# Kernel tuning notes

Measured on AMD Instinct MI355X. Metric: run time of the kernel, lower is better.

Reference implementation:

```python
import jax, jax.numpy as jnp
import numpy as np

S = 8192  # query length
T = 8192  # key/value length
D = 256   # head dim


def setup_inputs() -> dict:
    key = jax.random.key(0)
    kq, kk, kv = jax.random.split(key, 3)
    return {
        "query": jax.random.normal(kq, (S, D), dtype=jnp.float32),
        "key": jax.random.normal(kk, (T, D), dtype=jnp.float32),
        "value": jax.random.normal(kv, (T, D), dtype=jnp.float32),
    }


def reference(query, key, value):
    # attn_weights = Q @ K^T  (contract last dims, no batch dims)  -> [S, T]
    attn_weights = jnp.einsum("sd,td->st", query, key)
    # SoftmaxAttn: softmax over axes [ndim//2, ndim) == last axis for 2D
    attn_weights = jax.nn.softmax(attn_weights, axis=-1).astype(jnp.float32)
    # y = A @ V  -> [S, D]
    y = jnp.einsum("st,td->sd", attn_weights, value)
    return y
```

## Files before the change

kernel.cpp:

```cpp
#include <hip/hip_runtime.h>
#include <hip/hip_fp16.h>

#define S_LEN 8192
#define T_LEN 8192
#define D_DIM 256
#define QBLK 64
#define KVBLK 32
#define TSPLIT 8
#define NKV ((T_LEN / TSPLIT) / KVBLK)
#define NQT (S_LEN / QBLK)
#define KTILE_BYTES 16384
#define VTILE_BYTES 16384
#define RESCALE_THR 6.0f
#define LOG2E 1.44269504f

typedef _Float16 f16x8 __attribute__((ext_vector_type(8)));
typedef float f32x4 __attribute__((ext_vector_type(4)));

struct h4 { _Float16 h[4]; };

#define GLOAD_LDS16(g, l)                                              \
    __builtin_amdgcn_global_load_lds(                                  \
        (const __attribute__((address_space(1))) void*)(g),            \
        (__attribute__((address_space(3))) void*)(l), 16, 0, 0)

#define MFMA16(a, b, c) __builtin_amdgcn_mfma_f32_16x16x32_f16(a, b, c, 0, 0, 0)

#if __has_builtin(__builtin_amdgcn_exp2f)
#define EXP2(x) __builtin_amdgcn_exp2f(x)
#else
static __device__ __forceinline__ float EXP2(float x) {
    float y;
    asm("v_exp_f32 %0, %1" : "=v"(y) : "v"(x));
    return y;
}
#endif

__global__ __launch_bounds__(256) void cvt_kernel(const float* __restrict__ in,
                                                  _Float16* __restrict__ out, int n4) {
    int i = blockIdx.x * 256 + threadIdx.x;
    if (i < n4) {
        float4 v = ((const float4*)in)[i];
        h4 o;
        o.h[0] = (_Float16)(v.x * LOG2E); o.h[1] = (_Float16)(v.y * LOG2E);
        o.h[2] = (_Float16)(v.z * LOG2E); o.h[3] = (_Float16)(v.w * LOG2E);
        ((h4*)out)[i] = o;
    }
}

__global__ __launch_bounds__(256) void cvt_swz_kernel(const float* __restrict__ in,
                                                      _Float16* __restrict__ img,
                                                      int nchunks) {
    int id = blockIdx.x * 256 + threadIdx.x;
    if (id >= nchunks) return;
    int row = id >> 5, gr = id & 31;
    int t = row >> 5, r = row & 31;
    float4 a = *(const float4*)(in + (size_t)row * D_DIM + gr * 8);
    float4 b = *(const float4*)(in + (size_t)row * D_DIM + gr * 8 + 4);
    f16x8 o;
    o[0] = (_Float16)a.x; o[1] = (_Float16)a.y; o[2] = (_Float16)a.z; o[3] = (_Float16)a.w;
    o[4] = (_Float16)b.x; o[5] = (_Float16)b.y; o[6] = (_Float16)b.z; o[7] = (_Float16)b.w;
    *(f16x8*)((char*)img + (size_t)t * KTILE_BYTES + (gr >> 2) * 2048 +
              ((r >> 4) << 10) + ((r & 15) << 6) + ((gr & 3) << 4)) = o;
}

__global__ __launch_bounds__(256) void vt_swz_kernel(const float* __restrict__ V,
                                                     _Float16* __restrict__ Vimg) {
    __shared__ float tile[32][260];
    const int t = blockIdx.x;
#pragma unroll
    for (int i = 0; i < 8; ++i) {
        int idx = i * 256 + threadIdx.x;
        int kr = idx >> 6, c4 = idx & 63;
        float4 v = *(const float4*)(V + ((size_t)t * 32 + kr) * D_DIM + c4 * 4);
        tile[kr][c4 * 4 + 0] = v.x;
        tile[kr][c4 * 4 + 1] = v.y;
        tile[kr][c4 * 4 + 2] = v.z;
        tile[kr][c4 * 4 + 3] = v.w;
    }
    __syncthreads();
#pragma unroll
    for (int i = 0; i < 4; ++i) {
        int gid = i * 256 + threadIdx.x;
        int d = gid >> 2, gk = gid & 3;
        f16x8 o;
#pragma unroll
        for (int j = 0; j < 8; ++j)
            o[j] = (_Float16)tile[(j >> 2) * 16 + gk * 4 + (j & 3)][d];
        *(f16x8*)((char*)Vimg + (size_t)t * VTILE_BYTES + ((d >> 4) << 10) +
                  (gk << 8) + ((d & 15) << 4)) = o;
    }
}

__global__ __launch_bounds__(128, 2) void attn_kernel(
    const _Float16* __restrict__ Qh, const _Float16* __restrict__ Kimg,
    const _Float16* __restrict__ Vimg, _Float16* __restrict__ Opart,
    float* __restrict__ ml) {
    __shared__ __align__(16) char smem[32768];
    char* sK = smem;
    char* sV = smem + 16384;
    const int tid = threadIdx.x;
    const int wave = tid >> 6, lane = tid & 63;
    const int g = lane >> 4, c = lane & 15;
    const int qtile = blockIdx.x, split = blockIdx.y;
    const int tile0 = split * NKV;
    const int othr = tid * 16;
    const int kbase = ((lane & 15) << 6) | ((lane >> 4) << 4);
    const int vbase = lane << 4;

    f16x8 qf[2][8];
    {
        const size_t qrow0 = (size_t)qtile * QBLK + wave * 32 + c;
#pragma unroll
        for (int mi = 0; mi < 2; ++mi)
#pragma unroll
            for (int ks = 0; ks < 8; ++ks)
                qf[mi][ks] =
                    *(const f16x8*)(Qh + (qrow0 + mi * 16) * D_DIM + (ks * 4 + g) * 8);
    }

    {
        const char* Kt = (const char*)Kimg + (size_t)tile0 * KTILE_BYTES;
#pragma unroll
        for (int i = 0; i < 8; ++i) GLOAD_LDS16(Kt + i * 2048 + othr, sK + i * 2048 + othr);
    }

    f32x4 acc[2][16];
#pragma unroll
    for (int mi = 0; mi < 2; ++mi)
#pragma unroll
        for (int dt = 0; dt < 16; ++dt) acc[mi][dt] = (f32x4){0.f, 0.f, 0.f, 0.f};
    float m[2] = {-1e30f, -1e30f};
    float l[2] = {0.f, 0.f};

    for (int kt = 0; kt < NKV; ++kt) {
        asm volatile("s_waitcnt vmcnt(0)" ::: "memory");
        __builtin_amdgcn_s_barrier();

        {
            const char* Vt = (const char*)Vimg + (size_t)(tile0 + kt) * VTILE_BYTES;
#pragma unroll
            for (int i = 0; i < 8; ++i)
                GLOAD_LDS16(Vt + i * 2048 + othr, sV + i * 2048 + othr);
        }

        f32x4 st[2][2];
#pragma unroll
        for (int mi = 0; mi < 2; ++mi)
#pragma unroll
            for (int ct = 0; ct < 2; ++ct) st[mi][ct] = (f32x4){0.f, 0.f, 0.f, 0.f};
        __builtin_amdgcn_s_setprio(1);
#pragma unroll
        for (int ks = 0; ks < 8; ++ks) {
            f16x8 kf0 = *(const f16x8*)(sK + ks * 2048 + kbase);
            f16x8 kf1 = *(const f16x8*)(sK + ks * 2048 + 1024 + kbase);
            st[0][0] = MFMA16(kf0, qf[0][ks], st[0][0]);
            st[0][1] = MFMA16(kf1, qf[0][ks], st[0][1]);
            st[1][0] = MFMA16(kf0, qf[1][ks], st[1][0]);
            st[1][1] = MFMA16(kf1, qf[1][ks], st[1][1]);
        }
        __builtin_amdgcn_s_setprio(0);

        union PU { unsigned int u[4]; f16x8 v; };
        PU pu[2];
#pragma unroll
        for (int mi = 0; mi < 2; ++mi) {
            float pm = fmaxf(fmaxf(fmaxf(st[mi][0][0], st[mi][0][1]),
                                   fmaxf(st[mi][0][2], st[mi][0][3])),
                             fmaxf(fmaxf(st[mi][1][0], st[mi][1][1]),
                                   fmaxf(st[mi][1][2], st[mi][1][3])));
            if (__any(pm > m[mi] + RESCALE_THR)) {
                pm = fmaxf(pm, __shfl_xor(pm, 16));
                pm = fmaxf(pm, __shfl_xor(pm, 32));
                float mn = fmaxf(m[mi], pm);
                float sc = EXP2(m[mi] - mn);
                m[mi] = mn;
                l[mi] *= sc;
                float fr[4];
#pragma unroll
                for (int r = 0; r < 4; ++r) fr[r] = __shfl(sc, (g << 4) | (g * 4 + r));
#pragma unroll
                for (int dt = 0; dt < 16; ++dt)
#pragma unroll
                    for (int r = 0; r < 4; ++r) acc[mi][dt][r] *= fr[r];
            }
            float rs = 0.f;
#pragma unroll
            for (int ct = 0; ct < 2; ++ct)
#pragma unroll
                for (int r = 0; r < 4; ++r) {
                    float p = EXP2(st[mi][ct][r] - m[mi]);
                    st[mi][ct][r] = p;
                    rs += p;
                }
            l[mi] += rs;
            pu[mi].u[0] = __builtin_bit_cast(
                unsigned int, __builtin_amdgcn_cvt_pkrtz(st[mi][0][0], st[mi][0][1]));
            pu[mi].u[1] = __builtin_bit_cast(
                unsigned int, __builtin_amdgcn_cvt_pkrtz(st[mi][0][2], st[mi][0][3]));
            pu[mi].u[2] = __builtin_bit_cast(
                unsigned int, __builtin_amdgcn_cvt_pkrtz(st[mi][1][0], st[mi][1][1]));
            pu[mi].u[3] = __builtin_bit_cast(
                unsigned int, __builtin_amdgcn_cvt_pkrtz(st[mi][1][2], st[mi][1][3]));
        }

        asm volatile("s_waitcnt vmcnt(0)" ::: "memory");
        __builtin_amdgcn_s_barrier();

        if (kt + 1 < NKV) {
            const char* Kt = (const char*)Kimg + (size_t)(tile0 + kt + 1) * KTILE_BYTES;
#pragma unroll
            for (int i = 0; i < 8; ++i)
                GLOAD_LDS16(Kt + i * 2048 + othr, sK + i * 2048 + othr);
        }

        __builtin_amdgcn_s_setprio(1);
#pragma unroll
        for (int dt = 0; dt < 16; ++dt) {
            f16x8 vf = *(const f16x8*)(sV + dt * 1024 + vbase);
            acc[0][dt] = MFMA16(pu[0].v, vf, acc[0][dt]);
            acc[1][dt] = MFMA16(pu[1].v, vf, acc[1][dt]);
        }
        __builtin_amdgcn_s_setprio(0);
    }

    _Float16* Ob = Opart + (size_t)(qtile * TSPLIT + split) * QBLK * D_DIM;
#pragma unroll
    for (int mi = 0; mi < 2; ++mi)
#pragma unroll
        for (int dt = 0; dt < 16; ++dt)
#pragma unroll
            for (int r = 0; r < 4; ++r) {
                int row = wave * 32 + mi * 16 + g * 4 + r;
                int col = dt * 16 + c;
                Ob[(size_t)row * D_DIM + col] = (_Float16)acc[mi][dt][r];
            }
#pragma unroll
    for (int mi = 0; mi < 2; ++mi) {
        l[mi] += __shfl_xor(l[mi], 16);
        l[mi] += __shfl_xor(l[mi], 32);
    }
    if (g == 0) {
        float* mlb = ml + (size_t)((qtile * TSPLIT + split) * QBLK) * 2;
#pragma unroll
        for (int mi = 0; mi < 2; ++mi) {
            int row = wave * 32 + mi * 16 + c;
            mlb[row * 2 + 0] = m[mi];
            mlb[row * 2 + 1] = l[mi];
        }
    }
}

__global__ __launch_bounds__(256) void combine_kernel(const _Float16* __restrict__ Opart,
                                                      const float* __restrict__ ml,
                                                      float* __restrict__ out) {
    int r = blockIdx.x;
    int qtile = r >> 6, rl = r & 63;
    int d = threadIdx.x;
    float mv[TSPLIT], lv[TSPLIT];
    float M = -1e30f;
#pragma unroll
    for (int s = 0; s < TSPLIT; ++s) {
        const float* mlb = ml + (size_t)((qtile * TSPLIT + s) * QBLK + rl) * 2;
        mv[s] = mlb[0];
        lv[s] = mlb[1];
        M = fmaxf(M, mv[s]);
    }
    float num = 0.f, den = 0.f;
#pragma unroll
    for (int s = 0; s < TSPLIT; ++s) {
        float w = EXP2(mv[s] - M);
        num += w * (float)Opart[((size_t)(qtile * TSPLIT + s) * QBLK + rl) * D_DIM + d];
        den += w * lv[s];
    }
    out[(size_t)r * D_DIM + d] = num / den;
}

extern "C" void kernel_launch(void* const* d_in, const int* in_sizes, int n_in,
                              void* d_out, int out_size, void* d_ws, size_t ws_size,
                              hipStream_t stream) {
    const float* Q = (const float*)d_in[0];
    const float* K = (const float*)d_in[1];
    const float* V = (const float*)d_in[2];
    float* out = (float*)d_out;
    char* ws = (char*)d_ws;

    _Float16* Qh = (_Float16*)ws;
    _Float16* Kimg = (_Float16*)(ws + (4 << 20));
    _Float16* Vimg = (_Float16*)(ws + (8 << 20));
    _Float16* Opart = (_Float16*)(ws + (12 << 20));
    float* ml = (float*)(ws + ((size_t)44 << 20));

    const int n4 = S_LEN * D_DIM / 4;
    const int nchunks = S_LEN * D_DIM / 8;
    cvt_kernel<<<n4 / 256, 256, 0, stream>>>(Q, Qh, n4);
    cvt_swz_kernel<<<nchunks / 256, 256, 0, stream>>>(K, Kimg, nchunks);
    vt_swz_kernel<<<T_LEN / 32, 256, 0, stream>>>(V, Vimg);

    dim3 ag(NQT, TSPLIT);
    attn_kernel<<<ag, 128, 0, stream>>>(Qh, Kimg, Vimg, Opart, ml);
    combine_kernel<<<S_LEN, 256, 0, stream>>>(Opart, ml, out);
}
```

Before: 108.6 us.

## Double-buffer K/V tiles, widen Q block to 128 with rotated tile order

Raises the query block to 128 rows with 4 waves per block, so each K/V tile loaded to LDS serves twice as many queries. Replaces the serialized K-then-V load scheme with a double-buffered pipeline that prefetches the next K and V tiles together while computing the current one. Adds a per-qtile rotation of the KV tile start order and a 1D grid mapping, meant to spread concurrent block accesses across memory. LDS grows to 64KB per block, which may limit occupancy.

```diff
diff --git a/kernel.cpp b/kernel.cpp
--- a/kernel.cpp
+++ b/kernel.cpp
@@ -4,7 +4,7 @@
 #define S_LEN 8192
 #define T_LEN 8192
 #define D_DIM 256
-#define QBLK 64
+#define QBLK 128
 #define KVBLK 32
 #define TSPLIT 8
 #define NKV ((T_LEN / TSPLIT) / KVBLK)
@@ -92,18 +92,18 @@
     }
 }
 
-__global__ __launch_bounds__(128, 2) void attn_kernel(
+__global__ __launch_bounds__(256, 2) void attn_kernel(
     const _Float16* __restrict__ Qh, const _Float16* __restrict__ Kimg,
     const _Float16* __restrict__ Vimg, _Float16* __restrict__ Opart,
     float* __restrict__ ml) {
-    __shared__ __align__(16) char smem[32768];
-    char* sK = smem;
-    char* sV = smem + 16384;
+    __shared__ __align__(16) char smem[65536];
     const int tid = threadIdx.x;
     const int wave = tid >> 6, lane = tid & 63;
     const int g = lane >> 4, c = lane & 15;
-    const int qtile = blockIdx.x, split = blockIdx.y;
+    const int bid = blockIdx.x;
+    const int qtile = bid >> 3, split = bid & 7;
     const int tile0 = split * NKV;
+    const int rot = ((qtile >> 5) << 4) | ((qtile & 3) << 2);
     const int othr = tid * 16;
     const int kbase = ((lane & 15) << 6) | ((lane >> 4) << 4);
     const int vbase = lane << 4;
@@ -118,12 +118,7 @@
                 qf[mi][ks] =
                     *(const f16x8*)(Qh + (qrow0 + mi * 16) * D_DIM + (ks * 4 + g) * 8);
     }
-
-    {
-        const char* Kt = (const char*)Kimg + (size_t)tile0 * KTILE_BYTES;
-#pragma unroll
-        for (int i = 0; i < 8; ++i) GLOAD_LDS16(Kt + i * 2048 + othr, sK + i * 2048 + othr);
-    }
+    asm volatile("s_waitcnt vmcnt(0)" ::: "memory");
 
     f32x4 acc[2][16];
 #pragma unroll
@@ -133,16 +128,37 @@
     float m[2] = {-1e30f, -1e30f};
     float l[2] = {0.f, 0.f};
 
+    {
+        const int t0 = tile0 + rot;
+        const char* Kt = (const char*)Kimg + (size_t)t0 * KTILE_BYTES;
+        const char* Vt = (const char*)Vimg + (size_t)t0 * VTILE_BYTES;
+#pragma unroll
+        for (int i = 0; i < 4; ++i) {
+            GLOAD_LDS16(Kt + i * 4096 + othr, smem + i * 4096 + othr);
+            GLOAD_LDS16(Vt + i * 4096 + othr, smem + 32768 + i * 4096 + othr);
+        }
+    }
+
     for (int kt = 0; kt < NKV; ++kt) {
-        asm volatile("s_waitcnt vmcnt(0)" ::: "memory");
+        const int cur = kt & 1;
+        if (kt + 1 < NKV) {
+            const int tn = tile0 + ((kt + 1 + rot) & (NKV - 1));
+            const char* Kt = (const char*)Kimg + (size_t)tn * KTILE_BYTES;
+            const char* Vt = (const char*)Vimg + (size_t)tn * VTILE_BYTES;
+            const int nb = (cur ^ 1) * 16384;
+#pragma unroll
+            for (int i = 0; i < 4; ++i) {
+                GLOAD_LDS16(Kt + i * 4096 + othr, smem + nb + i * 4096 + othr);
+                GLOAD_LDS16(Vt + i * 4096 + othr, smem + 32768 + nb + i * 4096 + othr);
+            }
+            asm volatile("s_waitcnt vmcnt(8)" ::: "memory");
+        } else {
+            asm volatile("s_waitcnt vmcnt(0)" ::: "memory");
+        }
         __builtin_amdgcn_s_barrier();
 
-        {
-            const char* Vt = (const char*)Vimg + (size_t)(tile0 + kt) * VTILE_BYTES;
-#pragma unroll
-            for (int i = 0; i < 8; ++i)
-                GLOAD_LDS16(Vt + i * 2048 + othr, sV + i * 2048 + othr);
-        }
+        const char* sK = smem + cur * 16384;
+        const char* sV = smem + 32768 + cur * 16384;
 
         f32x4 st[2][2];
 #pragma unroll
@@ -204,16 +220,6 @@
                 unsigned int, __builtin_amdgcn_cvt_pkrtz(st[mi][1][2], st[mi][1][3]));
         }
 
-        asm volatile("s_waitcnt vmcnt(0)" ::: "memory");
-        __builtin_amdgcn_s_barrier();
-
-        if (kt + 1 < NKV) {
-            const char* Kt = (const char*)Kimg + (size_t)(tile0 + kt + 1) * KTILE_BYTES;
-#pragma unroll
-            for (int i = 0; i < 8; ++i)
-                GLOAD_LDS16(Kt + i * 2048 + othr, sK + i * 2048 + othr);
-        }
-
         __builtin_amdgcn_s_setprio(1);
 #pragma unroll
         for (int dt = 0; dt < 16; ++dt) {
@@ -222,6 +228,8 @@
             acc[1][dt] = MFMA16(pu[1].v, vf, acc[1][dt]);
         }
         __builtin_amdgcn_s_setprio(0);
+
+        __builtin_amdgcn_s_barrier();
     }
 
     _Float16* Ob = Opart + (size_t)(qtile * TSPLIT + split) * QBLK * D_DIM;
@@ -255,7 +263,7 @@
                                                       const float* __restrict__ ml,
                                                       float* __restrict__ out) {
     int r = blockIdx.x;
-    int qtile = r >> 6, rl = r & 63;
+    int qtile = r >> 7, rl = r & 127;
     int d = threadIdx.x;
     float mv[TSPLIT], lv[TSPLIT];
     float M = -1e30f;
@@ -297,7 +305,6 @@
     cvt_swz_kernel<<<nchunks / 256, 256, 0, stream>>>(K, Kimg, nchunks);
     vt_swz_kernel<<<T_LEN / 32, 256, 0, stream>>>(V, Vimg);
 
-    dim3 ag(NQT, TSPLIT);
-    attn_kernel<<<ag, 128, 0, stream>>>(Qh, Kimg, Vimg, Opart, ml);
+    attn_kernel<<<NQT * TSPLIT, 256, 0, stream>>>(Qh, Kimg, Vimg, Opart, ml);
     combine_kernel<<<S_LEN, 256, 0, stream>>>(Opart, ml, out);
 }
```

Result: faster. 105.0 us (-3.3%).

## Warp-specialize attention into QK/softmax producer and PV consumer waves

Applied to the files above, without the earlier changes.

Splits each 256-thread block into two producer waves that compute QK^T and softmax and two consumer waves that do the P·V accumulation. P tiles and rescale factors pass between the groups through double-buffered LDS, and K and V tiles are double-buffered. TSPLIT is halved, and each block rotates its KV tile order to spread L2 traffic. The aim is to overlap exp/softmax work with PV MFMAs and to cut the amount of partial output the combine step must process. In exchange it uses about 74 KB of dynamic LDS per block and adds barrier coupling between the two wave groups.

```diff
diff --git a/kernel.cpp b/kernel.cpp
--- a/kernel.cpp
+++ b/kernel.cpp
@@ -6,13 +6,14 @@
 #define D_DIM 256
 #define QBLK 64
 #define KVBLK 32
-#define TSPLIT 8
+#define TSPLIT 4
 #define NKV ((T_LEN / TSPLIT) / KVBLK)
 #define NQT (S_LEN / QBLK)
 #define KTILE_BYTES 16384
 #define VTILE_BYTES 16384
 #define RESCALE_THR 6.0f
 #define LOG2E 1.44269504f
+#define SMEM_BYTES 75776
 
 typedef _Float16 f16x8 __attribute__((ext_vector_type(8)));
 typedef float f32x4 __attribute__((ext_vector_type(4)));
@@ -92,162 +93,257 @@
     }
 }
 
-__global__ __launch_bounds__(128, 2) void attn_kernel(
+__global__ __launch_bounds__(256, 2) void attn_kernel(
     const _Float16* __restrict__ Qh, const _Float16* __restrict__ Kimg,
     const _Float16* __restrict__ Vimg, _Float16* __restrict__ Opart,
     float* __restrict__ ml) {
-    __shared__ __align__(16) char smem[32768];
+    extern __shared__ __align__(16) char smem[];
     char* sK = smem;
-    char* sV = smem + 16384;
+    char* sV = smem + 32768;
+    char* sPu = smem + 65536;
+    char* sSc = smem + 73728;
+
     const int tid = threadIdx.x;
     const int wave = tid >> 6, lane = tid & 63;
     const int g = lane >> 4, c = lane & 15;
-    const int qtile = blockIdx.x, split = blockIdx.y;
+    const int bid = blockIdx.x;
+    const int qtile = bid >> 2, split = bid & 3;
     const int tile0 = split * NKV;
-    const int othr = tid * 16;
-    const int kbase = ((lane & 15) << 6) | ((lane >> 4) << 4);
-    const int vbase = lane << 4;
-
-    f16x8 qf[2][8];
-    {
-        const size_t qrow0 = (size_t)qtile * QBLK + wave * 32 + c;
+    const int rot = ((qtile >> 6) << 5) | ((qtile & 7) << 2);
+
+    if (wave < 2) {
+        f16x8 qf[2][8];
+        {
+            const size_t qrow0 = (size_t)qtile * QBLK + wave * 32 + c;
+#pragma unroll
+            for (int mi = 0; mi < 2; ++mi)
+#pragma unroll
+                for (int ks = 0; ks < 8; ++ks)
+                    qf[mi][ks] = *(const f16x8*)(Qh + (qrow0 + mi * 16) * D_DIM +
+                                                 (ks * 4 + g) * 8);
+        }
+        asm volatile("s_waitcnt vmcnt(0)" ::: "memory");
+
+        {
+            const char* Kt =
+                (const char*)Kimg + (size_t)(tile0 + rot) * KTILE_BYTES;
+#pragma unroll
+            for (int i = 0; i < 8; ++i)
+                GLOAD_LDS16(Kt + i * 2048 + tid * 16, sK + i * 2048 + tid * 16);
+        }
+
+        const int kbase = (c << 6) | (g << 4);
+        float m[2] = {-1e30f, -1e30f};
+        float l[2] = {0.f, 0.f};
+
+        for (int kt = 0; kt < NKV; ++kt) {
+            asm volatile("s_waitcnt vmcnt(0)" ::: "memory");
+            __builtin_amdgcn_s_barrier();
+            if (kt + 1 < NKV) {
+                const int tn = tile0 + ((kt + 1 + rot) & (NKV - 1));
+                const char* Kt = (const char*)Kimg + (size_t)tn * KTILE_BYTES;
+                const int nb = ((kt + 1) & 1) * 16384;
+#pragma unroll
+                for (int i = 0; i < 8; ++i)
+                    GLOAD_LDS16(Kt + i * 2048 + tid * 16, sK + nb + i * 2048 + tid * 16);
+            }
+            const char* sKb = sK + (kt & 1) * 16384;
+
+            f32x4 st[2][2];
+#pragma unroll
+            for (int mi = 0; mi < 2; ++mi)
+#pragma unroll
+                for (int ct = 0; ct < 2; ++ct) st[mi][ct] = (f32x4){0.f, 0.f, 0.f, 0.f};
+            __builtin_amdgcn_s_setprio(1);
+#pragma unroll
+            for (int ks = 0; ks < 8; ++ks) {
+                f16x8 kf0 = *(const f16x8*)(sKb + ks * 2048 + kbase);
+                f16x8 kf1 = *(const f16x8*)(sKb + ks * 2048 + 1024 + kbase);
+                st[0][0] = MFMA16(kf0, qf[0][ks], st[0][0]);
+                st[0][1] = MFMA16(kf1, qf[0][ks], st[0][1]);
+                st[1][0] = MFMA16(kf0, qf[1][ks], st[1][0]);
+                st[1][1] = MFMA16(kf1, qf[1][ks], st[1][1]);
+            }
+            __builtin_amdgcn_s_setprio(0);
+
+            float sc[2];
+            uint4 pu[2];
+#pragma unroll
+            for (int mi = 0; mi < 2; ++mi) {
+                float pm = fmaxf(fmaxf(fmaxf(st[mi][0][0], st[mi][0][1]),
+                                       fmaxf(st[mi][0][2], st[mi][0][3])),
+                                 fmaxf(fmaxf(st[mi][1][0], st[mi][1][1]),
+                                       fmaxf(st[mi][1][2], st[mi][1][3])));
+                sc[mi] = 1.0f;
+                if (__any(pm > m[mi] + RESCALE_THR)) {
+                    pm = fmaxf(pm, __shfl_xor(pm, 16));
+                    pm = fmaxf(pm, __shfl_xor(pm, 32));
+                    float mn = fmaxf(m[mi], pm);
+                    sc[mi] = EXP2(m[mi] - mn);
+                    m[mi] = mn;
+                    l[mi] *= sc[mi];
+                }
+                float rs = 0.f;
+#pragma unroll
+                for (int ct = 0; ct < 2; ++ct)
+#pragma unroll
+                    for (int r = 0; r < 4; ++r) {
+                        float p = EXP2(st[mi][ct][r] - m[mi]);
+                        st[mi][ct][r] = p;
+                        rs += p;
+                    }
+                l[mi] += rs;
+                pu[mi].x = __builtin_bit_cast(
+                    unsigned int, __builtin_amdgcn_cvt_pkrtz(st[mi][0][0], st[mi][0][1]));
+                pu[mi].y = __builtin_bit_cast(
+                    unsigned int, __builtin_amdgcn_cvt_pkrtz(st[mi][0][2], st[mi][0][3]));
+                pu[mi].z = __builtin_bit_cast(
+                    unsigned int, __builtin_amdgcn_cvt_pkrtz(st[mi][1][0], st[mi][1][1]));
+                pu[mi].w = __builtin_bit_cast(
+                    unsigned int, __builtin_amdgcn_cvt_pkrtz(st[mi][1][2], st[mi][1][3]));
+            }
+
+            {
+                char* pb = sPu + (kt & 1) * 4096 + wave * 2048;
+                *(uint4*)(pb + lane * 16) = pu[0];
+                *(uint4*)(pb + 1024 + lane * 16) = pu[1];
+                *(float2*)(sSc + (kt & 1) * 1024 + wave * 512 + lane * 8) =
+                    make_float2(sc[0], sc[1]);
+            }
+            asm volatile("s_waitcnt lgkmcnt(0)" ::: "memory");
+            __builtin_amdgcn_sched_barrier(0);
+            __builtin_amdgcn_s_barrier();
+        }
+
+#pragma unroll
+        for (int mi = 0; mi < 2; ++mi) {
+            l[mi] += __shfl_xor(l[mi], 16);
+            l[mi] += __shfl_xor(l[mi], 32);
+        }
+        if (g == 0) {
+            float* mlb = ml + (size_t)((qtile * TSPLIT + split) * QBLK) * 2;
+#pragma unroll
+            for (int mi = 0; mi < 2; ++mi) {
+                int row = wave * 32 + mi * 16 + c;
+                mlb[row * 2 + 0] = m[mi];
+                mlb[row * 2 + 1] = l[mi];
+            }
+        }
+    } else {
+        const int ctid = tid - 128;
+        const int cw = wave - 2;
+        f32x4 acc[2][16];
 #pragma unroll
         for (int mi = 0; mi < 2; ++mi)
 #pragma unroll
-            for (int ks = 0; ks < 8; ++ks)
-                qf[mi][ks] =
-                    *(const f16x8*)(Qh + (qrow0 + mi * 16) * D_DIM + (ks * 4 + g) * 8);
-    }
-
-    {
-        const char* Kt = (const char*)Kimg + (size_t)tile0 * KTILE_BYTES;
-#pragma unroll
-        for (int i = 0; i < 8; ++i) GLOAD_LDS16(Kt + i * 2048 + othr, sK + i * 2048 + othr);
-    }
-
-    f32x4 acc[2][16];
-#pragma unroll
-    for (int mi = 0; mi < 2; ++mi)
-#pragma unroll
-        for (int dt = 0; dt < 16; ++dt) acc[mi][dt] = (f32x4){0.f, 0.f, 0.f, 0.f};
-    float m[2] = {-1e30f, -1e30f};
-    float l[2] = {0.f, 0.f};
-
-    for (int kt = 0; kt < NKV; ++kt) {
-        asm volatile("s_waitcnt vmcnt(0)" ::: "memory");
-        __builtin_amdgcn_s_barrier();
+            for (int dt = 0; dt < 16; ++dt) acc[mi][dt] = (f32x4){0.f, 0.f, 0.f, 0.f};
 
         {
-            const char* Vt = (const char*)Vimg + (size_t)(tile0 + kt) * VTILE_BYTES;
+            const char* Vt =
+                (const char*)Vimg + (size_t)(tile0 + rot) * VTILE_BYTES;
 #pragma unroll
             for (int i = 0; i < 8; ++i)
-                GLOAD_LDS16(Vt + i * 2048 + othr, sV + i * 2048 + othr);
-        }
-
-        f32x4 st[2][2];
+                GLOAD_LDS16(Vt + i * 2048 + ctid * 16, sV + i * 2048 + ctid * 16);
+        }
+
+        for (int kt = 0; kt < NKV; ++kt) {
+            __builtin_amdgcn_s_barrier();
+            if (kt > 0) {
+                const int j = kt - 1;
+                const char* sVb = sV + (j & 1) * 16384;
+                const char* pb = sPu + (j & 1) * 4096 + cw * 2048;
+                uint4 u0 = *(const uint4*)(pb + lane * 16);
+                uint4 u1 = *(const uint4*)(pb + 1024 + lane * 16);
+                float2 scv = *(const float2*)(sSc + (j & 1) * 1024 + cw * 512 + lane * 8);
+                if (__any(scv.x != 1.0f)) {
+                    float fr[4];
+#pragma unroll
+                    for (int r = 0; r < 4; ++r)
+                        fr[r] = __shfl(scv.x, (g << 4) | (g * 4 + r));
+#pragma unroll
+                    for (int dt = 0; dt < 16; ++dt)
+#pragma unroll
+                        for (int r = 0; r < 4; ++r) acc[0][dt][r] *= fr[r];
+                }
+                if (__any(scv.y != 1.0f)) {
+                    float fr[4];
+#pragma unroll
+                    for (int r = 0; r < 4; ++r)
+                        fr[r] = __shfl(scv.y, (g << 4) | (g * 4 + r));
+#pragma unroll
+                    for (int dt = 0; dt < 16; ++dt)
+#pragma unroll
+                        for (int r = 0; r < 4; ++r) acc[1][dt][r] *= fr[r];
+                }
+                f16x8 p0 = __builtin_bit_cast(f16x8, u0);
+                f16x8 p1 = __builtin_bit_cast(f16x8, u1);
+                __builtin_amdgcn_s_setprio(1);
+#pragma unroll
+                for (int dt = 0; dt < 16; ++dt) {
+                    f16x8 vf = *(const f16x8*)(sVb + dt * 1024 + lane * 16);
+                    acc[0][dt] = MFMA16(p0, vf, acc[0][dt]);
+                    acc[1][dt] = MFMA16(p1, vf, acc[1][dt]);
+                }
+                __builtin_amdgcn_s_setprio(0);
+            }
+            asm volatile("s_waitcnt vmcnt(0)" ::: "memory");
+            __builtin_amdgcn_s_barrier();
+            if (kt + 1 < NKV) {
+                const int tn = tile0 + ((kt + 1 + rot) & (NKV - 1));
+                const char* Vt = (const char*)Vimg + (size_t)tn * VTILE_BYTES;
+                const int nb = ((kt + 1) & 1) * 16384;
+#pragma unroll
+                for (int i = 0; i < 8; ++i)
+                    GLOAD_LDS16(Vt + i * 2048 + ctid * 16, sV + nb + i * 2048 + ctid * 16);
+            }
+        }
+
+        {
+            const int j = NKV - 1;
+            const char* sVb = sV + (j & 1) * 16384;
+            const char* pb = sPu + (j & 1) * 4096 + cw * 2048;
+            uint4 u0 = *(const uint4*)(pb + lane * 16);
+            uint4 u1 = *(const uint4*)(pb + 1024 + lane * 16);
+            float2 scv = *(const float2*)(sSc + (j & 1) * 1024 + cw * 512 + lane * 8);
+            if (__any(scv.x != 1.0f)) {
+                float fr[4];
+#pragma unroll
+                for (int r = 0; r < 4; ++r) fr[r] = __shfl(scv.x, (g << 4) | (g * 4 + r));
+#pragma unroll
+                for (int dt = 0; dt < 16; ++dt)
+#pragma unroll
+                    for (int r = 0; r < 4; ++r) acc[0][dt][r] *= fr[r];
+            }
+            if (__any(scv.y != 1.0f)) {
+                float fr[4];
+#pragma unroll
+                for (int r = 0; r < 4; ++r) fr[r] = __shfl(scv.y, (g << 4) | (g * 4 + r));
+#pragma unroll
+                for (int dt = 0; dt < 16; ++dt)
+#pragma unroll
+                    for (int r = 0; r < 4; ++r) acc[1][dt][r] *= fr[r];
+            }
+            f16x8 p0 = __builtin_bit_cast(f16x8, u0);
+            f16x8 p1 = __builtin_bit_cast(f16x8, u1);
+#pragma unroll
+            for (int dt = 0; dt < 16; ++dt) {
+                f16x8 vf = *(const f16x8*)(sVb + dt * 1024 + lane * 16);
+                acc[0][dt] = MFMA16(p0, vf, acc[0][dt]);
+                acc[1][dt] = MFMA16(p1, vf, acc[1][dt]);
+            }
+        }
+
+        _Float16* Ob = Opart + (size_t)(qtile * TSPLIT + split) * QBLK * D_DIM;
 #pragma unroll
         for (int mi = 0; mi < 2; ++mi)
 #pragma unroll
-            for (int ct = 0; ct < 2; ++ct) st[mi][ct] = (f32x4){0.f, 0.f, 0.f, 0.f};
-        __builtin_amdgcn_s_setprio(1);
-#pragma unroll
-        for (int ks = 0; ks < 8; ++ks) {
-            f16x8 kf0 = *(const f16x8*)(sK + ks * 2048 + kbase);
-            f16x8 kf1 = *(const f16x8*)(sK + ks * 2048 + 1024 + kbase);
-            st[0][0] = MFMA16(kf0, qf[0][ks], st[0][0]);
-            st[0][1] = MFMA16(kf1, qf[0][ks], st[0][1]);
-            st[1][0] = MFMA16(kf0, qf[1][ks], st[1][0]);
-            st[1][1] = MFMA16(kf1, qf[1][ks], st[1][1]);
-        }
-        __builtin_amdgcn_s_setprio(0);
-
-        union PU { unsigned int u[4]; f16x8 v; };
-        PU pu[2];
-#pragma unroll
-        for (int mi = 0; mi < 2; ++mi) {
-            float pm = fmaxf(fmaxf(fmaxf(st[mi][0][0], st[mi][0][1]),
-                                   fmaxf(st[mi][0][2], st[mi][0][3])),
-                             fmaxf(fmaxf(st[mi][1][0], st[mi][1][1]),
-                                   fmaxf(st[mi][1][2], st[mi][1][3])));
-            if (__any(pm > m[mi] + RESCALE_THR)) {
-                pm = fmaxf(pm, __shfl_xor(pm, 16));
-                pm = fmaxf(pm, __shfl_xor(pm, 32));
-                float mn = fmaxf(m[mi], pm);
-                float sc = EXP2(m[mi] - mn);
-                m[mi] = mn;
-                l[mi] *= sc;
-                float fr[4];
-#pragma unroll
-                for (int r = 0; r < 4; ++r) fr[r] = __shfl(sc, (g << 4) | (g * 4 + r));
-#pragma unroll
-                for (int dt = 0; dt < 16; ++dt)
-#pragma unroll
-                    for (int r = 0; r < 4; ++r) acc[mi][dt][r] *= fr[r];
-            }
-            float rs = 0.f;
-#pragma unroll
-            for (int ct = 0; ct < 2; ++ct)
+            for (int dt = 0; dt < 16; ++dt)
 #pragma unroll
                 for (int r = 0; r < 4; ++r) {
-                    float p = EXP2(st[mi][ct][r] - m[mi]);
-                    st[mi][ct][r] = p;
-                    rs += p;
-                }
-            l[mi] += rs;
-            pu[mi].u[0] = __builtin_bit_cast(
-                unsigned int, __builtin_amdgcn_cvt_pkrtz(st[mi][0][0], st[mi][0][1]));
-            pu[mi].u[1] = __builtin_bit_cast(
-                unsigned int, __builtin_amdgcn_cvt_pkrtz(st[mi][0][2], st[mi][0][3]));
-            pu[mi].u[2] = __builtin_bit_cast(
-                unsigned int, __builtin_amdgcn_cvt_pkrtz(st[mi][1][0], st[mi][1][1]));
-            pu[mi].u[3] = __builtin_bit_cast(
-                unsigned int, __builtin_amdgcn_cvt_pkrtz(st[mi][1][2], st[mi][1][3]));
-        }
-
-        asm volatile("s_waitcnt vmcnt(0)" ::: "memory");
-        __builtin_amdgcn_s_barrier();
-
-        if (kt + 1 < NKV) {
-            const char* Kt = (const char*)Kimg + (size_t)(tile0 + kt + 1) * KTILE_BYTES;
-#pragma unroll
-            for (int i = 0; i < 8; ++i)
-                GLOAD_LDS16(Kt + i * 2048 + othr, sK + i * 2048 + othr);
-        }
-
-        __builtin_amdgcn_s_setprio(1);
-#pragma unroll
-        for (int dt = 0; dt < 16; ++dt) {
-            f16x8 vf = *(const f16x8*)(sV + dt * 1024 + vbase);
-            acc[0][dt] = MFMA16(pu[0].v, vf, acc[0][dt]);
-            acc[1][dt] = MFMA16(pu[1].v, vf, acc[1][dt]);
-        }
-        __builtin_amdgcn_s_setprio(0);
-    }
-
-    _Float16* Ob = Opart + (size_t)(qtile * TSPLIT + split) * QBLK * D_DIM;
-#pragma unroll
-    for (int mi = 0; mi < 2; ++mi)
-#pragma unroll
-        for (int dt = 0; dt < 16; ++dt)
-#pragma unroll
-            for (int r = 0; r < 4; ++r) {
-                int row = wave * 32 + mi * 16 + g * 4 + r;
-                int col = dt * 16 + c;
-                Ob[(size_t)row * D_DIM + col] = (_Float16)acc[mi][dt][r];
-            }
-#pragma unroll
-    for (int mi = 0; mi < 2; ++mi) {
-        l[mi] += __shfl_xor(l[mi], 16);
-        l[mi] += __shfl_xor(l[mi], 32);
-    }
-    if (g == 0) {
-        float* mlb = ml + (size_t)((qtile * TSPLIT + split) * QBLK) * 2;
-#pragma unroll
-        for (int mi = 0; mi < 2; ++mi) {
-            int row = wave * 32 + mi * 16 + c;
-            mlb[row * 2 + 0] = m[mi];
-            mlb[row * 2 + 1] = l[mi];
-        }
+                    int row = cw * 32 + mi * 16 + g * 4 + r;
+                    int col = dt * 16 + c;
+                    Ob[(size_t)row * D_DIM + col] = (_Float16)acc[mi][dt][r];
+                }
     }
 }
 
@@ -289,7 +385,7 @@
     _Float16* Kimg = (_Float16*)(ws + (4 << 20));
     _Float16* Vimg = (_Float16*)(ws + (8 << 20));
     _Float16* Opart = (_Float16*)(ws + (12 << 20));
-    float* ml = (float*)(ws + ((size_t)44 << 20));
+    float* ml = (float*)(ws + ((size_t)28 << 20));
 
     const int n4 = S_LEN * D_DIM / 4;
     const int nchunks = S_LEN * D_DIM / 8;
@@ -297,7 +393,6 @@
     cvt_swz_kernel<<<nchunks / 256, 256, 0, stream>>>(K, Kimg, nchunks);
     vt_swz_kernel<<<T_LEN / 32, 256, 0, stream>>>(V, Vimg);
 
-    dim3 ag(NQT, TSPLIT);
-    attn_kernel<<<ag, 128, 0, stream>>>(Qh, Kimg, Vimg, Opart, ml);
+    attn_kernel<<<NQT * TSPLIT, 256, SMEM_BYTES, stream>>>(Qh, Kimg, Vimg, Opart, ml);
     combine_kernel<<<S_LEN, 256, 0, stream>>>(Opart, ml, out);
 }
```

Result: slower. 114.3 us (+5.3%).
